# Kernel optimization log

Measured on AMD Instinct MI355X. Metric: run time of the kernel, lower is better.

Reference implementation:

```python
import jax, jax.numpy as jnp
import numpy as np

B, T, H, IN, D = 256, 64, 256, 2, 8

def _gru_cell(x, h, Wih, Whh, bih, bhh):
    gi = x @ Wih.T + bih          # [B,3H]
    gh = h @ Whh.T + bhh
    ir, iz, inn = jnp.split(gi, 3, axis=-1)
    hr, hz, hn = jnp.split(gh, 3, axis=-1)
    r = jax.nn.sigmoid(ir + hr)
    z = jax.nn.sigmoid(iz + hz)
    n = jnp.tanh(inn + r * hn)
    return (1.0 - z) * n + z * h

def _gru2(x, h, p):
    # h: [2,B,H]; p: 8-tuple of layer-0 then layer-1 GRU params
    h0 = _gru_cell(x, h[0], p[0], p[1], p[2], p[3])
    h1 = _gru_cell(h0, h[1], p[4], p[5], p[6], p[7])
    return jnp.stack([h0, h1], axis=0)

def _attend(h_new, buf, i, attn_W, v_W, fc_W, fc_b):
    # h_new: [2,B,H] fresh RNN hidden; buf: [B,T,2,H] history of hiddens
    s = h_new.transpose(1, 0, 2)                            # [B,2,H]
    es = jnp.einsum('blh,gh->blg', s, attn_W[:, :H])        # s half of cat(s,hiddens)
    eh = jnp.einsum('bjlh,gh->bjlg', buf, attn_W[:, H:])    # hiddens half
    energy = jnp.tanh(es[:, None] + eh)                     # [B,T,2,H]
    logits = jnp.einsum('bjlg,og->bjlo', energy, v_W)       # [B,T,2,2]
    mask = (jnp.arange(buf.shape[1]) <= i)[None, :, None, None]
    logits = jnp.where(mask, logits, jnp.float32(-1e30))
    m = logits.max(axis=(1, 2), keepdims=True)              # softmax over all 2*(i+1) history slots
    e = jnp.exp(logits - m)
    a = e / e.sum(axis=(1, 2), keepdims=True)
    c = jnp.einsum('bjlo,bjlh->obh', a, buf)                # [2,B,H] == bmm(a,hiddens).transpose(0,1)
    h_cat = jnp.concatenate([c, h_new], axis=-1)            # [2,B,2H]
    return h_cat @ fc_W.T + fc_b                            # [2,B,H]

def setup_inputs():
    key = jax.random.key(0)
    ks = jax.random.split(key, 32)
    def u(k, shape, fan):
        b = 1.0 / np.sqrt(fan)
        return jax.random.uniform(k, shape, jnp.float32, -b, b)
    inp = {'received': jax.random.normal(ks[0], (B, T, IN), jnp.float32)}
    i = 1
    for g in ('g1', 'g2'):
        inp[g + '_Wih0'] = u(ks[i], (3 * H, IN), H); i += 1
        inp[g + '_Whh0'] = u(ks[i], (3 * H, H), H); i += 1
        inp[g + '_bih0'] = u(ks[i], (3 * H,), H); i += 1
        inp[g + '_bhh0'] = u(ks[i], (3 * H,), H); i += 1
        inp[g + '_Wih1'] = u(ks[i], (3 * H, H), H); i += 1
        inp[g + '_Whh1'] = u(ks[i], (3 * H, H), H); i += 1
        inp[g + '_bih1'] = u(ks[i], (3 * H,), H); i += 1
        inp[g + '_bhh1'] = u(ks[i], (3 * H,), H); i += 1
    inp['fc_W'] = u(ks[i], (H, 2 * H), 2 * H); i += 1
    inp['fc_b'] = u(ks[i], (H,), 2 * H); i += 1
    inp['attn_W'] = u(ks[i], (H, 2 * H), 2 * H); i += 1
    inp['v_W'] = u(ks[i], (2, H), H); i += 1
    inp['out_W'] = u(ks[i], (1, 2 * H), 2 * H); i += 1
    inp['out_b'] = u(ks[i], (1,), 2 * H); i += 1
    return inp

def reference(received, g1_Wih0, g1_Whh0, g1_bih0, g1_bhh0, g1_Wih1, g1_Whh1, g1_bih1, g1_bhh1,
              g2_Wih0, g2_Whh0, g2_bih0, g2_bhh0, g2_Wih1, g2_Whh1, g2_bih1, g2_bhh1,
              fc_W, fc_b, attn_W, v_W, out_W, out_b):
    p1 = (g1_Wih0, g1_Whh0, g1_bih0, g1_bhh0, g1_Wih1, g1_Whh1, g1_bih1, g1_bhh1)
    p2 = (g2_Wih0, g2_Whh0, g2_bih0, g2_bhh0, g2_Wih1, g2_Whh1, g2_bih1, g2_bhh1)
    b, t = received.shape[0], received.shape[1]
    h_init = jnp.zeros((2, b, H), received.dtype)
    buf_init = jnp.zeros((b, t, 2, H), received.dtype)

    def step(carry, inp):
        h1, h2, b1, b2 = carry
        x, i = inp
        h1n = _gru2(x, h1, p1)
        h2n = _gru2(x, h2, p2)
        b1 = b1.at[:, i].set(h1n.transpose(1, 0, 2))
        b2 = b2.at[:, i].set(h2n.transpose(1, 0, 2))
        h1a = _attend(h1n, b1, i, attn_W, v_W, fc_W, fc_b)
        h2a = _attend(h2n, b2, i, attn_W, v_W, fc_W, fc_b)
        return (h1a, h2a, b1, b2), (h1n[1], h2n[1])

    xs = (received.transpose(1, 0, 2), jnp.arange(t))
    _, (o1, o2) = jax.lax.scan(step, (h_init, h_init, buf_init, buf_init), xs)
    out1 = o1.transpose(1, 0, 2)   # [B,T,H] = concat of per-step top-layer GRU outputs
    out2 = o2.transpose(1, 0, 2)
    ar = jnp.arange(t)
    idx = jnp.where(ar >= t - D - 1, t - 1, ar + D)   # delayed stream-2 features
    rnn_out = jnp.concatenate([out1, out2[:, idx]], axis=-1)  # [B,T,2H]
    return jax.nn.sigmoid(rnn_out @ out_W.T + out_b)          # [B,T,1]
```

## Files before the change

### kernel.cpp

```cpp
#include <hip/hip_runtime.h>

#define BATCH 256
#define TT    64
#define HH    256
#define DD    8

#define BW    4
#define NTHR  512
#define NBLK  (2 * (BATCH / BW))

typedef __attribute__((ext_vector_type(8))) short bfrag;
typedef __attribute__((ext_vector_type(4))) float f4;
typedef __attribute__((ext_vector_type(4))) unsigned int uv4;
typedef __attribute__((ext_vector_type(2))) unsigned int uv2;

#define SWZ(g) ((((g) & 31) << 3) | ((g) >> 5))

__device__ __forceinline__ float rcpf(float x) { return __builtin_amdgcn_rcpf(x); }
__device__ __forceinline__ float sigf(float x) { return rcpf(1.0f + __expf(-x)); }
__device__ __forceinline__ float tanh_fast(float x) {
  const float e = __expf(-2.0f * x);
  return __builtin_fmaf(2.0f, rcpf(1.0f + e), -1.0f);
}
__device__ __forceinline__ unsigned short f2bf(float f) {
  union { float f; unsigned int u; } v; v.f = f;
  return (unsigned short)((v.u + 0x7fffu + ((v.u >> 16) & 1u)) >> 16);
}
__device__ __forceinline__ float bf_lo(unsigned int u) {
  union { unsigned int u; float f; } v; v.u = u << 16; return v.f;
}
__device__ __forceinline__ float bf_hi(unsigned int u) {
  union { unsigned int u; float f; } v; v.u = u & 0xffff0000u; return v.f;
}
__device__ __forceinline__ bfrag zero_frag() {
  bfrag r;
#pragma unroll
  for (int x = 0; x < 8; x++) r[x] = 0;
  return r;
}
__device__ __forceinline__ f4 mfma16(bfrag a, bfrag b, f4 c) {
  return __builtin_amdgcn_mfma_f32_16x16x32_bf16(a, b, c, 0, 0, 0);
}

#define W1_ELEMS  196608
#define STACK_W   (3 * W1_ELEMS)
#define B3_OFF    (2 * STACK_W)
#define B4_OFF    (B3_OFF + 131072)
#define WF_TOTAL  (B4_OFF + 131072)

__global__ __launch_bounds__(256) void prep_weights(
    const float* __restrict__ g1_Whh0, const float* __restrict__ g1_Wih1, const float* __restrict__ g1_Whh1,
    const float* __restrict__ g2_Whh0, const float* __restrict__ g2_Wih1, const float* __restrict__ g2_Whh1,
    const float* __restrict__ attn_W, const float* __restrict__ fc_W,
    unsigned short* __restrict__ wf) {
  const int id = blockIdx.x * 256 + threadIdx.x;
  if (id >= WF_TOTAL) return;
  float src;
  if (id < 2 * STACK_W) {
    const int s = id / STACK_W, r = id % STACK_W;
    const int mm = r / W1_ELEMS, e = r % W1_ELEMS;
    const int j = e & 7, lane = (e >> 3) & 63, c = (e >> 9) & 7, t = e >> 12;
    const int nt = t / 3, g = t % 3;
    const int n = nt * 16 + (lane & 15);
    const int k = c * 32 + ((lane >> 4) << 3) + j;
    const float* W = (mm == 0) ? (s ? g2_Whh0 : g1_Whh0)
                   : (mm == 1) ? (s ? g2_Wih1 : g1_Wih1)
                               : (s ? g2_Whh1 : g1_Whh1);
    src = W[(g * 256 + n) * 256 + k];
  } else if (id < B4_OFF) {
    const int e = id - B3_OFF;
    const int j = e & 7, lane = (e >> 3) & 63, c = (e >> 9) & 7, t = e >> 12;
    const int n = t * 16 + (lane & 15);
    const int k = c * 32 + ((lane >> 4) << 3) + j;
    src = (n < 256) ? attn_W[n * 512 + k] : attn_W[(n - 256) * 512 + 256 + k];
  } else {
    const int e = id - B4_OFF;
    const int j = e & 7, lane = (e >> 3) & 63, c = (e >> 9) & 15, t = e >> 13;
    const int n = t * 16 + (lane & 15);
    const int k = c * 32 + ((lane >> 4) << 3) + j;
    src = fc_W[n * 512 + k];
  }
  wf[id] = f2bf(src);
}

__global__ __launch_bounds__(NTHR, 2) void gru_attn(
    const float* __restrict__ received,
    const float* __restrict__ g1_Wih0, const float* __restrict__ g1_bih0, const float* __restrict__ g1_bhh0,
    const float* __restrict__ g1_bih1, const float* __restrict__ g1_bhh1,
    const float* __restrict__ g2_Wih0, const float* __restrict__ g2_bih0, const float* __restrict__ g2_bhh0,
    const float* __restrict__ g2_bih1, const float* __restrict__ g2_bhh1,
    const float* __restrict__ fc_b, const float* __restrict__ v_W, const float* __restrict__ out_W,
    const unsigned short* __restrict__ wf,
    unsigned short* __restrict__ buf_g, unsigned short* __restrict__ ehb_g,
    float* __restrict__ ws_p) {
  const int tid  = threadIdx.x;
  const int lane = tid & 63, wave = tid >> 6;
  const int col  = lane & 15, q = lane >> 4;
  const int s    = blockIdx.x & 1;
  const int b0   = (blockIdx.x >> 1) * BW;

  const float* Wih0 = s ? g2_Wih0 : g1_Wih0;
  const float* bih0 = s ? g2_bih0 : g1_bih0;
  const float* bhh0 = s ? g2_bhh0 : g1_bhh0;
  const float* bih1 = s ? g2_bih1 : g1_bih1;
  const float* bhh1 = s ? g2_bhh1 : g1_bhh1;

  const bfrag* W1  = (const bfrag*)(wf + (size_t)s * STACK_W);
  const bfrag* W2I = W1 + W1_ELEMS / 8;
  const bfrag* W2H = W2I + W1_ELEMS / 8;
  const bfrag* B3  = (const bfrag*)(wf + B3_OFF);
  const bfrag* B4  = (const bfrag*)(wf + B4_OFF);

  unsigned short* buf = buf_g + (size_t)s * BATCH * TT * 2 * HH;
  unsigned short* ehb = ehb_g + (size_t)s * BATCH * TT * 2 * HH;
  float* pp = ws_p + (size_t)s * BATCH * TT;

  float wxr0v[2], wxr1v[2], wxz0v[2], wxz1v[2], wxn0v[2], wxn1v[2];
  float br0v[2], bz0v[2], bni0v[2], bnh0v[2];
  float br1v[2], bz1v[2], bni1v[2], bnh1v[2];
  float fcbv[2], owvv[2];
#pragma unroll
  for (int r2 = 0; r2 < 2; r2++) {
    const int nm = (wave + 8 * r2) * 16 + col;
    wxr0v[r2] = Wih0[nm * 2];         wxr1v[r2] = Wih0[nm * 2 + 1];
    wxz0v[r2] = Wih0[(256 + nm) * 2]; wxz1v[r2] = Wih0[(256 + nm) * 2 + 1];
    wxn0v[r2] = Wih0[(512 + nm) * 2]; wxn1v[r2] = Wih0[(512 + nm) * 2 + 1];
    br0v[r2]  = bih0[nm] + bhh0[nm];
    bz0v[r2]  = bih0[256 + nm] + bhh0[256 + nm];
    bni0v[r2] = bih0[512 + nm]; bnh0v[r2] = bhh0[512 + nm];
    br1v[r2]  = bih1[nm] + bhh1[nm];
    bz1v[r2]  = bih1[256 + nm] + bhh1[256 + nm];
    bni1v[r2] = bih1[512 + nm]; bnh1v[r2] = bhh1[512 + nm];
    fcbv[r2]  = fc_b[nm];
    owvv[r2]  = out_W[s * HH + nm];
  }

  __shared__ float          hf[8 * 260] __attribute__((aligned(16)));
  __shared__ unsigned short hb[8 * 264] __attribute__((aligned(16)));
  __shared__ unsigned short hnb[8 * 264] __attribute__((aligned(16)));
  __shared__ float          es_s[8 * 264] __attribute__((aligned(16)));
  __shared__ unsigned short cacb[8 * 264] __attribute__((aligned(16)));
  __shared__ float          lp[TT * 4 * 2 * 2];
  __shared__ float          vw_s[512];
  __shared__ float          cpart[2 * 2 * 4 * 256] __attribute__((aligned(16)));
  __shared__ float          pw_s[32];
  __shared__ float          sinv_s[8];

  for (int x = tid; x < 8 * 260; x += NTHR) hf[x] = 0.0f;
  for (int x = tid; x < 8 * 264; x += NTHR) hb[x] = 0;
  { const int o = tid >> 8, g = tid & 255; vw_s[o * 256 + SWZ(g)] = v_W[tid]; }
  __syncthreads();

#pragma unroll 1
  for (int i = 0; i < TT; ++i) {
    float2 xv[BW];
#pragma unroll
    for (int b = 0; b < BW; b++) xv[b] = ((const float2*)received)[(size_t)(b0 + b) * TT + i];

    {
      bfrag a0[8];
#pragma unroll
      for (int c = 0; c < 8; c++)
        a0[c] = (col < BW) ? *(const bfrag*)&hb[col * 264 + c * 32 + q * 8] : zero_frag();
#pragma unroll
      for (int r2 = 0; r2 < 2; r2++) {
        const int nt16 = wave + 8 * r2;
        bfrag bb[24];
#pragma unroll
        for (int c = 0; c < 8; c++) {
          bb[c]      = W1[((nt16 * 3 + 0) * 8 + c) * 64 + lane];
          bb[8 + c]  = W1[((nt16 * 3 + 1) * 8 + c) * 64 + lane];
          bb[16 + c] = W1[((nt16 * 3 + 2) * 8 + c) * 64 + lane];
        }
        f4 aR = {0, 0, 0, 0}, aZ = {0, 0, 0, 0}, aN = {0, 0, 0, 0};
#pragma unroll
        for (int c = 0; c < 8; c++) {
          aR = mfma16(a0[c], bb[c], aR);
          aZ = mfma16(a0[c], bb[8 + c], aZ);
          aN = mfma16(a0[c], bb[16 + c], aN);
        }
        if (lane < 16) {
          const int nm = nt16 * 16 + col;
#pragma unroll
          for (int reg = 0; reg < 4; reg++) {
            const int b = reg;
            const float rr = sigf(xv[b].x * wxr0v[r2] + xv[b].y * wxr1v[r2] + br0v[r2] + aR[reg]);
            const float zz = sigf(xv[b].x * wxz0v[r2] + xv[b].y * wxz1v[r2] + bz0v[r2] + aZ[reg]);
            const float nn = tanh_fast(xv[b].x * wxn0v[r2] + xv[b].y * wxn1v[r2] + bni0v[r2] +
                                       rr * (aN[reg] + bnh0v[r2]));
            const float hn0 = (1.0f - zz) * nn + zz * hf[b * 260 + nm];
            const unsigned short hv = f2bf(hn0);
            hnb[b * 264 + nm] = hv;
            buf[((size_t)(b0 + b) * (TT * 2) + i * 2 + 0) * HH + nm] = hv;
          }
        }
      }
    }
    __syncthreads();

    {
      bfrag ai[8], ah[8];
#pragma unroll
      for (int c = 0; c < 8; c++) {
        ai[c] = (col < BW) ? *(const bfrag*)&hnb[col * 264 + c * 32 + q * 8] : zero_frag();
        ah[c] = (col < BW) ? *(const bfrag*)&hb[(4 + col) * 264 + c * 32 + q * 8] : zero_frag();
      }
      float pv[4] = {0.f, 0.f, 0.f, 0.f};
#pragma unroll
      for (int r2 = 0; r2 < 2; r2++) {
        const int nt16 = wave + 8 * r2;
        bfrag bb[24];
#pragma unroll
        for (int c = 0; c < 8; c++) {
          bb[c]      = W2I[((nt16 * 3 + 0) * 8 + c) * 64 + lane];
          bb[8 + c]  = W2I[((nt16 * 3 + 1) * 8 + c) * 64 + lane];
          bb[16 + c] = W2I[((nt16 * 3 + 2) * 8 + c) * 64 + lane];
        }
        f4 iR = {0, 0, 0, 0}, iZ = {0, 0, 0, 0}, iN = {0, 0, 0, 0};
#pragma unroll
        for (int c = 0; c < 8; c++) {
          iR = mfma16(ai[c], bb[c], iR);
          iZ = mfma16(ai[c], bb[8 + c], iZ);
          iN = mfma16(ai[c], bb[16 + c], iN);
        }
#pragma unroll
        for (int c = 0; c < 8; c++) {
          bb[c]      = W2H[((nt16 * 3 + 0) * 8 + c) * 64 + lane];
          bb[8 + c]  = W2H[((nt16 * 3 + 1) * 8 + c) * 64 + lane];
          bb[16 + c] = W2H[((nt16 * 3 + 2) * 8 + c) * 64 + lane];
        }
        f4 hR = {0, 0, 0, 0}, hZ = {0, 0, 0, 0}, hN = {0, 0, 0, 0};
#pragma unroll
        for (int c = 0; c < 8; c++) {
          hR = mfma16(ah[c], bb[c], hR);
          hZ = mfma16(ah[c], bb[8 + c], hZ);
          hN = mfma16(ah[c], bb[16 + c], hN);
        }
        if (lane < 16) {
          const int nm = nt16 * 16 + col;
#pragma unroll
          for (int reg = 0; reg < 4; reg++) {
            const int b = reg;
            const float rr = sigf(iR[reg] + hR[reg] + br1v[r2]);
            const float zz = sigf(iZ[reg] + hZ[reg] + bz1v[r2]);
            const float nn = tanh_fast(iN[reg] + bni1v[r2] + rr * (hN[reg] + bnh1v[r2]));
            const float hn1 = (1.0f - zz) * nn + zz * hf[(4 + b) * 260 + nm];
            const unsigned short hv = f2bf(hn1);
            hnb[(4 + b) * 264 + nm] = hv;
            buf[((size_t)(b0 + b) * (TT * 2) + i * 2 + 1) * HH + nm] = hv;
            pv[reg] += hn1 * owvv[r2];
          }
        }
      }
#pragma unroll
      for (int reg = 0; reg < 4; reg++) {
#pragma unroll
        for (int d = 1; d < 16; d <<= 1) pv[reg] += __shfl_xor(pv[reg], d, 64);
      }
      if (lane == 0) {
#pragma unroll
        for (int reg = 0; reg < 4; reg++) pw_s[wave * 4 + reg] = pv[reg];
      }
    }
    __syncthreads();

    {
      bfrag a3[8];
#pragma unroll
      for (int c = 0; c < 8; c++)
        a3[c] = (col < 8) ? *(const bfrag*)&hnb[col * 264 + c * 32 + q * 8] : zero_frag();
#pragma unroll
      for (int tt = 0; tt < 4; tt++) {
        const int t = wave * 4 + tt;
        bfrag bb[8];
#pragma unroll
        for (int c = 0; c < 8; c++) bb[c] = B3[(t * 8 + c) * 64 + lane];
        f4 acc = {0, 0, 0, 0};
#pragma unroll
        for (int c = 0; c < 8; c++) acc = mfma16(a3[c], bb[c], acc);
        if (lane < 32) {
          const int n = t * 16 + col;
#pragma unroll
          for (int reg = 0; reg < 4; reg++) {
            const int m = q * 4 + reg;
            const int l = m >> 2, b = m & 3;
            if (t < 16) es_s[(b * 2 + l) * 264 + SWZ(n)] = acc[reg];
            else ehb[((size_t)(b0 + b) * (TT * 2) + i * 2 + l) * HH + (n - 256)] = f2bf(acc[reg]);
          }
        }
      }
      if (tid < 4) {
        float ss = 0.0f;
#pragma unroll
        for (int w = 0; w < 8; w++) ss += pw_s[w * 4 + tid];
        pp[(size_t)(b0 + tid) * TT + i] = ss;
      }
    }
    __syncthreads();

    {
      const int nslot = 64 * (i + 1);
      int slot = tid;
      uv4 cur[4];
      if (slot < nslot) {
        const uv4* ep = (const uv4*)(ehb + ((size_t)(b0 + ((slot >> 3) & 3)) * (TT * 2) +
                                            (slot >> 6) * 2 + ((slot >> 5) & 1)) * HH + (slot & 7) * 32);
#pragma unroll
        for (int u = 0; u < 4; u++) cur[u] = __builtin_nontemporal_load(ep + u);
      }
      for (; slot < nslot; slot += NTHR) {
        const int snext = slot + NTHR;
        uv4 nxt[4];
        if (snext < nslot) {
          const uv4* ep2 = (const uv4*)(ehb + ((size_t)(b0 + ((snext >> 3) & 3)) * (TT * 2) +
                                               (snext >> 6) * 2 + ((snext >> 5) & 1)) * HH + (snext & 7) * 32);
#pragma unroll
          for (int u = 0; u < 4; u++) nxt[u] = __builtin_nontemporal_load(ep2 + u);
        } else {
#pragma unroll
          for (int u = 0; u < 4; u++) nxt[u] = cur[u];
        }
        const int g8 = slot & 7;
        const int b  = (slot >> 3) & 3;
        const int l  = (slot >> 5) & 1;
        const int j  = slot >> 6;
        const int eb = (b * 2 + l) * 264;
        float l0 = 0.0f, l1 = 0.0f;
#pragma unroll
        for (int u = 0; u < 4; u++) {
#pragma unroll
          for (int k = 0; k < 4; k++) {
            const int m = u * 8 + k * 2;
            const float e0 = tanh_fast(es_s[eb + (m * 8 + g8)] + bf_lo(cur[u][k]));
            const float e1 = tanh_fast(es_s[eb + ((m + 1) * 8 + g8)] + bf_hi(cur[u][k]));
            l0 = fmaf(e0, vw_s[m * 8 + g8], fmaf(e1, vw_s[(m + 1) * 8 + g8], l0));
            l1 = fmaf(e0, vw_s[256 + m * 8 + g8], fmaf(e1, vw_s[256 + (m + 1) * 8 + g8], l1));
          }
        }
#pragma unroll
        for (int d = 1; d < 8; d <<= 1) { l0 += __shfl_xor(l0, d, 64); l1 += __shfl_xor(l1, d, 64); }
        if (g8 == 0) {
          lp[((j * 4 + b) * 2 + l) * 2 + 0] = __expf(l0);
          lp[((j * 4 + b) * 2 + l) * 2 + 1] = __expf(l1);
        }
#pragma unroll
        for (int u = 0; u < 4; u++) cur[u] = nxt[u];
      }
    }
    __syncthreads();

    {
      {
        const int b = wave >> 1, o = wave & 1;
        const int jl2 = 2 * (i + 1);
        const int jl0 = lane, jl1 = lane + 64;
        float sa = 0.0f;
        if (jl0 < jl2) sa += lp[((jl0 >> 1) * 4 + b) * 4 + (jl0 & 1) * 2 + o];
        if (jl1 < jl2) sa += lp[((jl1 >> 1) * 4 + b) * 4 + (jl1 & 1) * 2 + o];
#pragma unroll
        for (int d = 1; d < 64; d <<= 1) sa += __shfl_xor(sa, d, 64);
        if (lane == 0) sinv_s[b * 2 + o] = rcpf(sa);
      }
      const int h4   = tid & 63;
      const int jpar = (tid >> 6) & 1;
      const int cb   = tid >> 7;
      const uv2* bp = (const uv2*)(buf + ((size_t)(b0 + cb) * (TT * 2)) * HH);
      float c00 = 0.f, c01 = 0.f, c02 = 0.f, c03 = 0.f;
      float c10 = 0.f, c11 = 0.f, c12 = 0.f, c13 = 0.f;
      uv2 aj0 = {0, 0}, aj1 = {0, 0}, bj0 = {0, 0}, bj1 = {0, 0};
      int j = jpar;
      if (j <= i) {
        aj0 = __builtin_nontemporal_load(bp + (j * 2 + 0) * 64 + h4);
        aj1 = __builtin_nontemporal_load(bp + (j * 2 + 1) * 64 + h4);
        bj0 = __builtin_nontemporal_load(bp + ((j + 2) * 2 + 0) * 64 + h4);
        bj1 = __builtin_nontemporal_load(bp + ((j + 2) * 2 + 1) * 64 + h4);
      }
      for (; j <= i; j += 2) {
        uv2 cj0 = {0, 0}, cj1 = {0, 0};
        if (j + 4 <= i) {
          cj0 = __builtin_nontemporal_load(bp + ((j + 4) * 2 + 0) * 64 + h4);
          cj1 = __builtin_nontemporal_load(bp + ((j + 4) * 2 + 1) * 64 + h4);
        }
#pragma unroll
        for (int l = 0; l < 2; l++) {
          const uv2 u = l ? aj1 : aj0;
          const float e0 = lp[((j * 4 + cb) * 2 + l) * 2 + 0];
          const float e1 = lp[((j * 4 + cb) * 2 + l) * 2 + 1];
          const float v0 = bf_lo(u[0]), v1 = bf_hi(u[0]);
          const float v2 = bf_lo(u[1]), v3 = bf_hi(u[1]);
          c00 = fmaf(e0, v0, c00); c01 = fmaf(e0, v1, c01);
          c02 = fmaf(e0, v2, c02); c03 = fmaf(e0, v3, c03);
          c10 = fmaf(e1, v0, c10); c11 = fmaf(e1, v1, c11);
          c12 = fmaf(e1, v2, c12); c13 = fmaf(e1, v3, c13);
        }
        aj0 = bj0; aj1 = bj1; bj0 = cj0; bj1 = cj1;
      }
      ((float4*)&cpart[((jpar * 2 + 0) * 4 + cb) * 256])[h4] = make_float4(c00, c01, c02, c03);
      ((float4*)&cpart[((jpar * 2 + 1) * 4 + cb) * 256])[h4] = make_float4(c10, c11, c12, c13);
    }
    __syncthreads();

    for (int x = tid; x < 2 * BW * HH; x += NTHR) {
      const int g = x & 255, b = (x >> 8) & 3, o = x >> 10;
      const float v = (cpart[(o * 4 + b) * 256 + g] + cpart[((2 + o) * 4 + b) * 256 + g]) *
                      sinv_s[b * 2 + o];
      cacb[(o * 4 + b) * 264 + g] = f2bf(v);
    }
    __syncthreads();

    {
      bfrag a4[16];
      if (col < 8) {
#pragma unroll
        for (int c = 0; c < 8; c++) {
          a4[c]     = *(const bfrag*)&cacb[col * 264 + c * 32 + q * 8];
          a4[c + 8] = *(const bfrag*)&hnb[col * 264 + c * 32 + q * 8];
        }
      } else {
#pragma unroll
        for (int c = 0; c < 16; c++) a4[c] = zero_frag();
      }
#pragma unroll
      for (int r2 = 0; r2 < 2; r2++) {
        const int t16 = wave + 8 * r2;
        bfrag bb[16];
#pragma unroll
        for (int c = 0; c < 16; c++) bb[c] = B4[(t16 * 16 + c) * 64 + lane];
        f4 acc = {0, 0, 0, 0};
#pragma unroll
        for (int c = 0; c < 16; c++) acc = mfma16(a4[c], bb[c], acc);
        if (lane < 32) {
          const int nm = t16 * 16 + col;
#pragma unroll
          for (int reg = 0; reg < 4; reg++) {
            const int m = q * 4 + reg;
            const float v = acc[reg] + fcbv[r2];
            hf[m * 260 + nm] = v;
            hb[m * 264 + nm] = f2bf(v);
          }
        }
      }
    }
    __syncthreads();
  }
}

__global__ __launch_bounds__(256) void final_combine(const float* __restrict__ ws_p,
                                                     const float* __restrict__ out_b,
                                                     float* __restrict__ out) {
  const int gidx = blockIdx.x * blockDim.x + threadIdx.x;
  if (gidx >= BATCH * TT) return;
  const int b = gidx >> 6;
  const int t = gidx & 63;
  const int idx = (t >= TT - DD - 1) ? (TT - 1) : (t + DD);
  const float* p1 = ws_p;
  const float* p2 = ws_p + (size_t)BATCH * TT;
  const float v = p1[(size_t)b * TT + t] + p2[(size_t)b * TT + idx] + out_b[0];
  out[gidx] = 1.0f / (1.0f + __expf(-v));
}

extern "C" void kernel_launch(void* const* d_in, const int* in_sizes, int n_in,
                              void* d_out, int out_size, void* d_ws, size_t ws_size,
                              hipStream_t stream) {
  const float* received = (const float*)d_in[0];
  const float* g1_Wih0 = (const float*)d_in[1];
  const float* g1_Whh0 = (const float*)d_in[2];
  const float* g1_bih0 = (const float*)d_in[3];
  const float* g1_bhh0 = (const float*)d_in[4];
  const float* g1_Wih1 = (const float*)d_in[5];
  const float* g1_Whh1 = (const float*)d_in[6];
  const float* g1_bih1 = (const float*)d_in[7];
  const float* g1_bhh1 = (const float*)d_in[8];
  const float* g2_Wih0 = (const float*)d_in[9];
  const float* g2_Whh0 = (const float*)d_in[10];
  const float* g2_bih0 = (const float*)d_in[11];
  const float* g2_bhh0 = (const float*)d_in[12];
  const float* g2_Wih1 = (const float*)d_in[13];
  const float* g2_Whh1 = (const float*)d_in[14];
  const float* g2_bih1 = (const float*)d_in[15];
  const float* g2_bhh1 = (const float*)d_in[16];
  const float* fc_W   = (const float*)d_in[17];
  const float* fc_b   = (const float*)d_in[18];
  const float* attn_W = (const float*)d_in[19];
  const float* v_W    = (const float*)d_in[20];
  const float* out_W  = (const float*)d_in[21];
  const float* out_b  = (const float*)d_in[22];

  float* ws_p = (float*)d_ws;
  unsigned short* buf = (unsigned short*)(ws_p + 2 * BATCH * TT);
  unsigned short* ehb = buf + (size_t)2 * BATCH * TT * 2 * HH;
  unsigned short* wf  = ehb + (size_t)2 * BATCH * TT * 2 * HH;

  hipLaunchKernelGGL(prep_weights, dim3((WF_TOTAL + 255) / 256), dim3(256), 0, stream,
                     g1_Whh0, g1_Wih1, g1_Whh1, g2_Whh0, g2_Wih1, g2_Whh1,
                     attn_W, fc_W, wf);

  hipLaunchKernelGGL(gru_attn, dim3(NBLK), dim3(NTHR), 0, stream,
                     received,
                     g1_Wih0, g1_bih0, g1_bhh0, g1_bih1, g1_bhh1,
                     g2_Wih0, g2_bih0, g2_bhh0, g2_bih1, g2_bhh1,
                     fc_b, v_W, out_W, wf, buf, ehb, ws_p);

  hipLaunchKernelGGL(final_combine, dim3((BATCH * TT + 255) / 256), dim3(256), 0, stream,
                     ws_p, out_b, (float*)d_out);
}
```

Before: 6.879 ms.

## Double block size to 1024 threads with one output tile per wave

```diff
diff --git a/kernel.cpp b/kernel.cpp
--- a/kernel.cpp
+++ b/kernel.cpp
@@ -6,7 +6,7 @@
 #define DD    8
 
 #define BW    4
-#define NTHR  512
+#define NTHR  1024
 #define NBLK  (2 * (BATCH / BW))
 
 typedef __attribute__((ext_vector_type(8))) short bfrag;
@@ -83,7 +83,7 @@
   wf[id] = f2bf(src);
 }
 
-__global__ __launch_bounds__(NTHR, 2) void gru_attn(
+__global__ __launch_bounds__(NTHR, 4) void gru_attn(
     const float* __restrict__ received,
     const float* __restrict__ g1_Wih0, const float* __restrict__ g1_bih0, const float* __restrict__ g1_bhh0,
     const float* __restrict__ g1_bih1, const float* __restrict__ g1_bhh1,
@@ -115,25 +115,18 @@
   unsigned short* ehb = ehb_g + (size_t)s * BATCH * TT * 2 * HH;
   float* pp = ws_p + (size_t)s * BATCH * TT;
 
-  float wxr0v[2], wxr1v[2], wxz0v[2], wxz1v[2], wxn0v[2], wxn1v[2];
-  float br0v[2], bz0v[2], bni0v[2], bnh0v[2];
-  float br1v[2], bz1v[2], bni1v[2], bnh1v[2];
-  float fcbv[2], owvv[2];
-#pragma unroll
-  for (int r2 = 0; r2 < 2; r2++) {
-    const int nm = (wave + 8 * r2) * 16 + col;
-    wxr0v[r2] = Wih0[nm * 2];         wxr1v[r2] = Wih0[nm * 2 + 1];
-    wxz0v[r2] = Wih0[(256 + nm) * 2]; wxz1v[r2] = Wih0[(256 + nm) * 2 + 1];
-    wxn0v[r2] = Wih0[(512 + nm) * 2]; wxn1v[r2] = Wih0[(512 + nm) * 2 + 1];
-    br0v[r2]  = bih0[nm] + bhh0[nm];
-    bz0v[r2]  = bih0[256 + nm] + bhh0[256 + nm];
-    bni0v[r2] = bih0[512 + nm]; bnh0v[r2] = bhh0[512 + nm];
-    br1v[r2]  = bih1[nm] + bhh1[nm];
-    bz1v[r2]  = bih1[256 + nm] + bhh1[256 + nm];
-    bni1v[r2] = bih1[512 + nm]; bnh1v[r2] = bhh1[512 + nm];
-    fcbv[r2]  = fc_b[nm];
-    owvv[r2]  = out_W[s * HH + nm];
-  }
+  const int nm0 = wave * 16 + col;
+  const float wxr0 = Wih0[nm0 * 2],         wxr1 = Wih0[nm0 * 2 + 1];
+  const float wxz0 = Wih0[(256 + nm0) * 2], wxz1 = Wih0[(256 + nm0) * 2 + 1];
+  const float wxn0 = Wih0[(512 + nm0) * 2], wxn1 = Wih0[(512 + nm0) * 2 + 1];
+  const float br0  = bih0[nm0] + bhh0[nm0];
+  const float bz0  = bih0[256 + nm0] + bhh0[256 + nm0];
+  const float bni0 = bih0[512 + nm0], bnh0 = bhh0[512 + nm0];
+  const float br1  = bih1[nm0] + bhh1[nm0];
+  const float bz1  = bih1[256 + nm0] + bhh1[256 + nm0];
+  const float bni1 = bih1[512 + nm0], bnh1 = bhh1[512 + nm0];
+  const float fcb  = fc_b[nm0];
+  const float owv  = out_W[s * HH + nm0];
 
   __shared__ float          hf[8 * 260] __attribute__((aligned(16)));
   __shared__ unsigned short hb[8 * 264] __attribute__((aligned(16)));
@@ -142,13 +135,13 @@
   __shared__ unsigned short cacb[8 * 264] __attribute__((aligned(16)));
   __shared__ float          lp[TT * 4 * 2 * 2];
   __shared__ float          vw_s[512];
-  __shared__ float          cpart[2 * 2 * 4 * 256] __attribute__((aligned(16)));
-  __shared__ float          pw_s[32];
+  __shared__ float          cpart[4 * 2 * 4 * 256] __attribute__((aligned(16)));
+  __shared__ float          pw_s[64];
   __shared__ float          sinv_s[8];
 
   for (int x = tid; x < 8 * 260; x += NTHR) hf[x] = 0.0f;
   for (int x = tid; x < 8 * 264; x += NTHR) hb[x] = 0;
-  { const int o = tid >> 8, g = tid & 255; vw_s[o * 256 + SWZ(g)] = v_W[tid]; }
+  if (tid < 512) { const int o = tid >> 8, g = tid & 255; vw_s[o * 256 + SWZ(g)] = v_W[tid]; }
   __syncthreads();
 
 #pragma unroll 1
@@ -162,37 +155,33 @@
 #pragma unroll
       for (int c = 0; c < 8; c++)
         a0[c] = (col < BW) ? *(const bfrag*)&hb[col * 264 + c * 32 + q * 8] : zero_frag();
-#pragma unroll
-      for (int r2 = 0; r2 < 2; r2++) {
-        const int nt16 = wave + 8 * r2;
-        bfrag bb[24];
-#pragma unroll
-        for (int c = 0; c < 8; c++) {
-          bb[c]      = W1[((nt16 * 3 + 0) * 8 + c) * 64 + lane];
-          bb[8 + c]  = W1[((nt16 * 3 + 1) * 8 + c) * 64 + lane];
-          bb[16 + c] = W1[((nt16 * 3 + 2) * 8 + c) * 64 + lane];
-        }
-        f4 aR = {0, 0, 0, 0}, aZ = {0, 0, 0, 0}, aN = {0, 0, 0, 0};
-#pragma unroll
-        for (int c = 0; c < 8; c++) {
-          aR = mfma16(a0[c], bb[c], aR);
-          aZ = mfma16(a0[c], bb[8 + c], aZ);
-          aN = mfma16(a0[c], bb[16 + c], aN);
-        }
-        if (lane < 16) {
-          const int nm = nt16 * 16 + col;
-#pragma unroll
-          for (int reg = 0; reg < 4; reg++) {
-            const int b = reg;
-            const float rr = sigf(xv[b].x * wxr0v[r2] + xv[b].y * wxr1v[r2] + br0v[r2] + aR[reg]);
-            const float zz = sigf(xv[b].x * wxz0v[r2] + xv[b].y * wxz1v[r2] + bz0v[r2] + aZ[reg]);
-            const float nn = tanh_fast(xv[b].x * wxn0v[r2] + xv[b].y * wxn1v[r2] + bni0v[r2] +
-                                       rr * (aN[reg] + bnh0v[r2]));
-            const float hn0 = (1.0f - zz) * nn + zz * hf[b * 260 + nm];
-            const unsigned short hv = f2bf(hn0);
-            hnb[b * 264 + nm] = hv;
-            buf[((size_t)(b0 + b) * (TT * 2) + i * 2 + 0) * HH + nm] = hv;
-          }
+      const int nt16 = wave;
+      bfrag bb[24];
+#pragma unroll
+      for (int c = 0; c < 8; c++) {
+        bb[c]      = W1[((nt16 * 3 + 0) * 8 + c) * 64 + lane];
+        bb[8 + c]  = W1[((nt16 * 3 + 1) * 8 + c) * 64 + lane];
+        bb[16 + c] = W1[((nt16 * 3 + 2) * 8 + c) * 64 + lane];
+      }
+      f4 aR = {0, 0, 0, 0}, aZ = {0, 0, 0, 0}, aN = {0, 0, 0, 0};
+#pragma unroll
+      for (int c = 0; c < 8; c++) {
+        aR = mfma16(a0[c], bb[c], aR);
+        aZ = mfma16(a0[c], bb[8 + c], aZ);
+        aN = mfma16(a0[c], bb[16 + c], aN);
+      }
+      if (lane < 16) {
+#pragma unroll
+        for (int reg = 0; reg < 4; reg++) {
+          const int b = reg;
+          const float rr = sigf(xv[b].x * wxr0 + xv[b].y * wxr1 + br0 + aR[reg]);
+          const float zz = sigf(xv[b].x * wxz0 + xv[b].y * wxz1 + bz0 + aZ[reg]);
+          const float nn = tanh_fast(xv[b].x * wxn0 + xv[b].y * wxn1 + bni0 +
+                                     rr * (aN[reg] + bnh0));
+          const float hn0 = (1.0f - zz) * nn + zz * hf[b * 260 + nm0];
+          const unsigned short hv = f2bf(hn0);
+          hnb[b * 264 + nm0] = hv;
+          buf[((size_t)(b0 + b) * (TT * 2) + i * 2 + 0) * HH + nm0] = hv;
         }
       }
     }
@@ -206,50 +195,46 @@
         ah[c] = (col < BW) ? *(const bfrag*)&hb[(4 + col) * 264 + c * 32 + q * 8] : zero_frag();
       }
       float pv[4] = {0.f, 0.f, 0.f, 0.f};
-#pragma unroll
-      for (int r2 = 0; r2 < 2; r2++) {
-        const int nt16 = wave + 8 * r2;
-        bfrag bb[24];
-#pragma unroll
-        for (int c = 0; c < 8; c++) {
-          bb[c]      = W2I[((nt16 * 3 + 0) * 8 + c) * 64 + lane];
-          bb[8 + c]  = W2I[((nt16 * 3 + 1) * 8 + c) * 64 + lane];
-          bb[16 + c] = W2I[((nt16 * 3 + 2) * 8 + c) * 64 + lane];
-        }
-        f4 iR = {0, 0, 0, 0}, iZ = {0, 0, 0, 0}, iN = {0, 0, 0, 0};
-#pragma unroll
-        for (int c = 0; c < 8; c++) {
-          iR = mfma16(ai[c], bb[c], iR);
-          iZ = mfma16(ai[c], bb[8 + c], iZ);
-          iN = mfma16(ai[c], bb[16 + c], iN);
-        }
-#pragma unroll
-        for (int c = 0; c < 8; c++) {
-          bb[c]      = W2H[((nt16 * 3 + 0) * 8 + c) * 64 + lane];
-          bb[8 + c]  = W2H[((nt16 * 3 + 1) * 8 + c) * 64 + lane];
-          bb[16 + c] = W2H[((nt16 * 3 + 2) * 8 + c) * 64 + lane];
-        }
-        f4 hR = {0, 0, 0, 0}, hZ = {0, 0, 0, 0}, hN = {0, 0, 0, 0};
-#pragma unroll
-        for (int c = 0; c < 8; c++) {
-          hR = mfma16(ah[c], bb[c], hR);
-          hZ = mfma16(ah[c], bb[8 + c], hZ);
-          hN = mfma16(ah[c], bb[16 + c], hN);
-        }
-        if (lane < 16) {
-          const int nm = nt16 * 16 + col;
-#pragma unroll
-          for (int reg = 0; reg < 4; reg++) {
-            const int b = reg;
-            const float rr = sigf(iR[reg] + hR[reg] + br1v[r2]);
-            const float zz = sigf(iZ[reg] + hZ[reg] + bz1v[r2]);
-            const float nn = tanh_fast(iN[reg] + bni1v[r2] + rr * (hN[reg] + bnh1v[r2]));
-            const float hn1 = (1.0f - zz) * nn + zz * hf[(4 + b) * 260 + nm];
-            const unsigned short hv = f2bf(hn1);
-            hnb[(4 + b) * 264 + nm] = hv;
-            buf[((size_t)(b0 + b) * (TT * 2) + i * 2 + 1) * HH + nm] = hv;
-            pv[reg] += hn1 * owvv[r2];
-          }
+      const int nt16 = wave;
+      bfrag bb[24];
+#pragma unroll
+      for (int c = 0; c < 8; c++) {
+        bb[c]      = W2I[((nt16 * 3 + 0) * 8 + c) * 64 + lane];
+        bb[8 + c]  = W2I[((nt16 * 3 + 1) * 8 + c) * 64 + lane];
+        bb[16 + c] = W2I[((nt16 * 3 + 2) * 8 + c) * 64 + lane];
+      }
+      f4 iR = {0, 0, 0, 0}, iZ = {0, 0, 0, 0}, iN = {0, 0, 0, 0};
+#pragma unroll
+      for (int c = 0; c < 8; c++) {
+        iR = mfma16(ai[c], bb[c], iR);
+        iZ = mfma16(ai[c], bb[8 + c], iZ);
+        iN = mfma16(ai[c], bb[16 + c], iN);
+      }
+#pragma unroll
+      for (int c = 0; c < 8; c++) {
+        bb[c]      = W2H[((nt16 * 3 + 0) * 8 + c) * 64 + lane];
+        bb[8 + c]  = W2H[((nt16 * 3 + 1) * 8 + c) * 64 + lane];
+        bb[16 + c] = W2H[((nt16 * 3 + 2) * 8 + c) * 64 + lane];
+      }
+      f4 hR = {0, 0, 0, 0}, hZ = {0, 0, 0, 0}, hN = {0, 0, 0, 0};
+#pragma unroll
+      for (int c = 0; c < 8; c++) {
+        hR = mfma16(ah[c], bb[c], hR);
+        hZ = mfma16(ah[c], bb[8 + c], hZ);
+        hN = mfma16(ah[c], bb[16 + c], hN);
+      }
+      if (lane < 16) {
+#pragma unroll
+        for (int reg = 0; reg < 4; reg++) {
+          const int b = reg;
+          const float rr = sigf(iR[reg] + hR[reg] + br1);
+          const float zz = sigf(iZ[reg] + hZ[reg] + bz1);
+          const float nn = tanh_fast(iN[reg] + bni1 + rr * (hN[reg] + bnh1));
+          const float hn1 = (1.0f - zz) * nn + zz * hf[(4 + b) * 260 + nm0];
+          const unsigned short hv = f2bf(hn1);
+          hnb[(4 + b) * 264 + nm0] = hv;
+          buf[((size_t)(b0 + b) * (TT * 2) + i * 2 + 1) * HH + nm0] = hv;
+          pv[reg] += hn1 * owv;
         }
       }
 #pragma unroll
@@ -270,8 +255,8 @@
       for (int c = 0; c < 8; c++)
         a3[c] = (col < 8) ? *(const bfrag*)&hnb[col * 264 + c * 32 + q * 8] : zero_frag();
 #pragma unroll
-      for (int tt = 0; tt < 4; tt++) {
-        const int t = wave * 4 + tt;
+      for (int tt = 0; tt < 2; tt++) {
+        const int t = wave * 2 + tt;
         bfrag bb[8];
 #pragma unroll
         for (int c = 0; c < 8; c++) bb[c] = B3[(t * 8 + c) * 64 + lane];
@@ -292,7 +277,7 @@
       if (tid < 4) {
         float ss = 0.0f;
 #pragma unroll
-        for (int w = 0; w < 8; w++) ss += pw_s[w * 4 + tid];
+        for (int w = 0; w < 16; w++) ss += pw_s[w * 4 + tid];
         pp[(size_t)(b0 + tid) * TT + i] = ss;
       }
     }
@@ -350,7 +335,7 @@
     __syncthreads();
 
     {
-      {
+      if (wave < 8) {
         const int b = wave >> 1, o = wave & 1;
         const int jl2 = 2 * (i + 1);
         const int jl0 = lane, jl1 = lane + 64;
@@ -362,8 +347,8 @@
         if (lane == 0) sinv_s[b * 2 + o] = rcpf(sa);
       }
       const int h4   = tid & 63;
-      const int jpar = (tid >> 6) & 1;
-      const int cb   = tid >> 7;
+      const int jpar = (tid >> 6) & 3;
+      const int cb   = tid >> 8;
       const uv2* bp = (const uv2*)(buf + ((size_t)(b0 + cb) * (TT * 2)) * HH);
       float c00 = 0.f, c01 = 0.f, c02 = 0.f, c03 = 0.f;
       float c10 = 0.f, c11 = 0.f, c12 = 0.f, c13 = 0.f;
@@ -372,14 +357,14 @@
       if (j <= i) {
         aj0 = __builtin_nontemporal_load(bp + (j * 2 + 0) * 64 + h4);
         aj1 = __builtin_nontemporal_load(bp + (j * 2 + 1) * 64 + h4);
-        bj0 = __builtin_nontemporal_load(bp + ((j + 2) * 2 + 0) * 64 + h4);
-        bj1 = __builtin_nontemporal_load(bp + ((j + 2) * 2 + 1) * 64 + h4);
-      }
-      for (; j <= i; j += 2) {
+        bj0 = __builtin_nontemporal_load(bp + ((j + 4) * 2 + 0) * 64 + h4);
+        bj1 = __builtin_nontemporal_load(bp + ((j + 4) * 2 + 1) * 64 + h4);
+      }
+      for (; j <= i; j += 4) {
         uv2 cj0 = {0, 0}, cj1 = {0, 0};
-        if (j + 4 <= i) {
-          cj0 = __builtin_nontemporal_load(bp + ((j + 4) * 2 + 0) * 64 + h4);
-          cj1 = __builtin_nontemporal_load(bp + ((j + 4) * 2 + 1) * 64 + h4);
+        if (j + 8 <= i) {
+          cj0 = __builtin_nontemporal_load(bp + ((j + 8) * 2 + 0) * 64 + h4);
+          cj1 = __builtin_nontemporal_load(bp + ((j + 8) * 2 + 1) * 64 + h4);
         }
 #pragma unroll
         for (int l = 0; l < 2; l++) {
@@ -402,7 +387,10 @@
 
     for (int x = tid; x < 2 * BW * HH; x += NTHR) {
       const int g = x & 255, b = (x >> 8) & 3, o = x >> 10;
-      const float v = (cpart[(o * 4 + b) * 256 + g] + cpart[((2 + o) * 4 + b) * 256 + g]) *
+      const float v = (cpart[((0 * 2 + o) * 4 + b) * 256 + g] +
+                       cpart[((1 * 2 + o) * 4 + b) * 256 + g] +
+                       cpart[((2 * 2 + o) * 4 + b) * 256 + g] +
+                       cpart[((3 * 2 + o) * 4 + b) * 256 + g]) *
                       sinv_s[b * 2 + o];
       cacb[(o * 4 + b) * 264 + g] = f2bf(v);
     }
@@ -420,24 +408,20 @@
 #pragma unroll
         for (int c = 0; c < 16; c++) a4[c] = zero_frag();
       }
-#pragma unroll
-      for (int r2 = 0; r2 < 2; r2++) {
-        const int t16 = wave + 8 * r2;
-        bfrag bb[16];
-#pragma unroll
-        for (int c = 0; c < 16; c++) bb[c] = B4[(t16 * 16 + c) * 64 + lane];
-        f4 acc = {0, 0, 0, 0};
-#pragma unroll
-        for (int c = 0; c < 16; c++) acc = mfma16(a4[c], bb[c], acc);
-        if (lane < 32) {
-          const int nm = t16 * 16 + col;
-#pragma unroll
-          for (int reg = 0; reg < 4; reg++) {
-            const int m = q * 4 + reg;
-            const float v = acc[reg] + fcbv[r2];
-            hf[m * 260 + nm] = v;
-            hb[m * 264 + nm] = f2bf(v);
-          }
+      const int t16 = wave;
+      bfrag bb[16];
+#pragma unroll
+      for (int c = 0; c < 16; c++) bb[c] = B4[(t16 * 16 + c) * 64 + lane];
+      f4 acc = {0, 0, 0, 0};
+#pragma unroll
+      for (int c = 0; c < 16; c++) acc = mfma16(a4[c], bb[c], acc);
+      if (lane < 32) {
+#pragma unroll
+        for (int reg = 0; reg < 4; reg++) {
+          const int m = q * 4 + reg;
+          const float v = acc[reg] + fcb;
+          hf[m * 260 + nm0] = v;
+          hb[m * 264 + nm0] = f2bf(v);
         }
       }
     }
```

Result: faster. 5.618 ms (-18.3%).
